# Kernel tuning notes

Hardware: AMD Instinct MI355X
Metric: run time of the kernel (lower is better)

The kernel has to match this reference:

```python
import jax, jax.numpy as jnp
import numpy as np

B, S, E, H = 1, 2048, 1024, 16
D = E // H
HEAVY_RATIO, RECENT_RATIO, PENALTY = 0.1, 0.1, 0.99
NEG = jnp.finfo(jnp.float32).min


def heavy_hitter_mask(attn, heavy_budget, recent_budget, penalty):
    # attn: [N, S, S] pre-softmax scores (with causal mask already added)
    N, Sq, _ = attn.shape
    cb = heavy_budget + recent_budget  # cache budget
    cols = jnp.arange(Sq)
    tmp = jax.nn.softmax(attn.astype(jnp.float32), axis=-1)
    # exponential penalty factor: penalty ** (cb-1, cb-2, ..., 0)
    pf = penalty ** (jnp.arange(cb, 0, -1).astype(jnp.float32) - 1.0)
    acc = jnp.einsum('nts,t->ns', tmp[:, :cb, :], pf)  # accumulated attention score [N,S]
    acc = acc * (cols < cb).astype(jnp.float32)        # zero beyond cache budget
    prev0 = jnp.broadcast_to(cols < cb, (N, Sq))       # mask_bottom row cb-1 (pre-tril)
    rows = jnp.swapaxes(attn[:, cb:, :], 0, 1)         # time-major [T,N,S]
    toks = jnp.arange(cb, Sq)

    def step(carry, inp):
        acc, prev = carry
        row, tok = inp
        li = tok - recent_budget                       # local_index
        in_local = (cols < li)[None, :]
        acc = jnp.where(in_local, acc * prev.astype(jnp.float32), acc)
        scores = jnp.where(in_local, acc, -jnp.inf)
        _, idx = jax.lax.top_k(scores, heavy_budget)   # heavy hitters [N,k]
        heavy = jnp.zeros((N, Sq), bool).at[jnp.arange(N)[:, None], idx].set(True)
        mask_row = heavy | (cols >= li)[None, :]
        p = jax.nn.softmax(jnp.where(mask_row, row.astype(jnp.float32), NEG), axis=-1)
        acc = acc * penalty + p
        # carry pre-tril row (matches torch loop); emit tril'd row
        return (acc, mask_row), mask_row & (cols <= tok)[None, :]

    (_, _), out_rows = jax.lax.scan(step, (acc, prev0), (rows, toks))
    # first cb rows: all-True cb x cb block, then tril -> causal within block
    top = jnp.broadcast_to((cols[None, :] <= jnp.arange(cb)[:, None])[None], (N, cb, Sq))
    return jnp.concatenate([top, jnp.swapaxes(out_rows, 0, 1)], axis=1)


def _forward(hidden_states, attention_mask, Wq, bq, Wk, bk, Wv, bv, Wo, bo):
    scaling = D ** -0.5
    q = (hidden_states @ Wq.T + bq) * scaling
    k = hidden_states @ Wk.T + bk
    v = hidden_states @ Wv.T + bv

    def shp(x):
        return x.reshape(B, S, H, D).transpose(0, 2, 1, 3).reshape(B * H, S, D)

    q, k, v = shp(q), shp(k), shp(v)
    attn = jnp.einsum('nsd,ntd->nst', q, k)                    # [B*H,S,S]
    attn = attn.reshape(B, H, S, S) + attention_mask
    attn = jnp.maximum(attn, NEG).reshape(B * H, S, S)
    hb = int(HEAVY_RATIO * S)
    rb = int(RECENT_RATIO * S)
    mask = heavy_hitter_mask(attn, hb, rb, PENALTY)
    attn = jnp.where(mask, attn, jnp.min(attention_mask))
    probs = jax.nn.softmax(attn.astype(jnp.float32), axis=-1)
    out = jnp.einsum('nst,ntd->nsd', probs, v)
    out = out.reshape(B, H, S, D).transpose(0, 2, 1, 3).reshape(B, S, E)
    return out @ Wo.T + bo


def setup_inputs() -> dict:
    key = jax.random.key(0)
    ks = jax.random.split(key, 9)
    hidden_states = jax.random.normal(ks[0], (B, S, E), jnp.float32)
    cols = jnp.arange(S)
    causal = (cols[None, :] <= cols[:, None])
    attention_mask = jnp.where(causal, 0.0, NEG)[None, None].astype(jnp.float32)
    attention_mask = jnp.broadcast_to(attention_mask, (B, 1, S, S)) + jnp.zeros((B, 1, S, S), jnp.float32)
    lin = lambda k: jax.random.normal(k, (E, E), jnp.float32) * 0.02
    return {
        'hidden_states': hidden_states,
        'attention_mask': attention_mask,
        'Wq': lin(ks[1]), 'bq': jnp.zeros((E,), jnp.float32),
        'Wk': lin(ks[2]), 'bk': jnp.zeros((E,), jnp.float32),
        'Wv': lin(ks[3]), 'bv': jnp.zeros((E,), jnp.float32),
        'Wo': lin(ks[4]), 'bo': jnp.zeros((E,), jnp.float32),
    }


def reference(hidden_states, attention_mask, Wq, bq, Wk, bk, Wv, bv, Wo, bo):
    return _forward(hidden_states, attention_mask, Wq, bq, Wk, bk, Wv, bv, Wo, bo)
```

## Files before the change

### kernel.cpp

```cpp
#include <hip/hip_runtime.h>

#define S_ 2048
#define E_ 1024
#define H_ 16
#define D_ 64
#define HB_ 204
#define RB_ 204
#define CB_ 408
#define NSCAN_ (S_ - CB_)
#define PEN_ 0.99f
#define NEGINF (-__builtin_huge_valf())
#define POSINF (__builtin_huge_valf())

typedef unsigned short u16;
typedef unsigned int u32;
typedef unsigned int u32x4 __attribute__((ext_vector_type(4)));

__device__ __forceinline__ float bf2f(u16 u) {
    union { u32 u; float f; } a; a.u = ((u32)u) << 16; return a.f;
}
__device__ __forceinline__ u16 f2bf(float f) {
    union { float f; u32 u; } a; a.f = f;
    u32 r = (a.u + 0x7FFFu + ((a.u >> 16) & 1u)) >> 16;
    return (u16)r;
}

#define DPPF(ID, V, CTRL, RMASK) \
    __int_as_float(__builtin_amdgcn_update_dpp(__float_as_int(ID), __float_as_int(V), CTRL, RMASK, 0xf, false))

__device__ __forceinline__ float wsum64_63(float v) {
    float t;
    t = DPPF(0.f, v, 0x111, 0xf); v += t;
    t = DPPF(0.f, v, 0x112, 0xf); v += t;
    t = DPPF(0.f, v, 0x114, 0xf); v += t;
    t = DPPF(0.f, v, 0x118, 0xf); v += t;
    t = DPPF(0.f, v, 0x142, 0xa); v += t;
    t = DPPF(0.f, v, 0x143, 0xc); v += t;
    return v;
}
__device__ __forceinline__ float wsum64(float v) {
    v = wsum64_63(v);
    return __int_as_float(__builtin_amdgcn_readlane(__float_as_int(v), 63));
}
template <int CTRL, int RMASK>
__device__ __forceinline__ double dmin_step(double v) {
    const int lo = __double2loint(v), hi = __double2hiint(v);
    const int slo = __builtin_amdgcn_update_dpp(0, lo, CTRL, RMASK, 0xf, false);
    const int shi = __builtin_amdgcn_update_dpp(0x7FF00000, hi, CTRL, RMASK, 0xf, false);
    return fmin(v, __hiloint2double(shi, slo));
}
__device__ __forceinline__ double wmind64(double v) {
    v = dmin_step<0x111, 0xf>(v);
    v = dmin_step<0x112, 0xf>(v);
    v = dmin_step<0x114, 0xf>(v);
    v = dmin_step<0x118, 0xf>(v);
    v = dmin_step<0x142, 0xa>(v);
    v = dmin_step<0x143, 0xc>(v);
    return v;
}

__global__ __launch_bounds__(256) void qkv_gemm(
    const float* __restrict__ X,
    const float* __restrict__ W0, const float* __restrict__ b0,
    const float* __restrict__ W1, const float* __restrict__ b1,
    const float* __restrict__ W2, const float* __restrict__ b2,
    float* __restrict__ Q, float* __restrict__ K, float* __restrict__ V)
{
    const int z = blockIdx.z;
    const float* W    = (z == 0) ? W0 : (z == 1) ? W1 : W2;
    const float* bias = (z == 0) ? b0 : (z == 1) ? b1 : b2;
    float* dst        = (z == 0) ? Q  : (z == 1) ? K  : V;
    const int o0 = blockIdx.x * 128, s0 = blockIdx.y * 128;
    __shared__ float As[16][132];
    __shared__ float Bs[16][132];
    const int tid = threadIdx.x;
    const int ty = tid >> 4, tx = tid & 15;
    const int r = tid >> 1, kq = (tid & 1) << 3;
    float acc[8][8] = {};
    for (int kb = 0; kb < E_; kb += 16) {
        float4 a0 = *(const float4*)&X[(size_t)(s0 + r) * E_ + kb + kq];
        float4 a1 = *(const float4*)&X[(size_t)(s0 + r) * E_ + kb + kq + 4];
        float4 w0 = *(const float4*)&W[(size_t)(o0 + r) * E_ + kb + kq];
        float4 w1 = *(const float4*)&W[(size_t)(o0 + r) * E_ + kb + kq + 4];
        __syncthreads();
        As[kq+0][r]=a0.x; As[kq+1][r]=a0.y; As[kq+2][r]=a0.z; As[kq+3][r]=a0.w;
        As[kq+4][r]=a1.x; As[kq+5][r]=a1.y; As[kq+6][r]=a1.z; As[kq+7][r]=a1.w;
        Bs[kq+0][r]=w0.x; Bs[kq+1][r]=w0.y; Bs[kq+2][r]=w0.z; Bs[kq+3][r]=w0.w;
        Bs[kq+4][r]=w1.x; Bs[kq+5][r]=w1.y; Bs[kq+6][r]=w1.z; Bs[kq+7][r]=w1.w;
        __syncthreads();
        #pragma unroll
        for (int kk = 0; kk < 16; ++kk) {
            float av[8], bv[8];
            *(float4*)&av[0] = *(const float4*)&As[kk][ty * 8];
            *(float4*)&av[4] = *(const float4*)&As[kk][ty * 8 + 4];
            *(float4*)&bv[0] = *(const float4*)&Bs[kk][tx * 8];
            *(float4*)&bv[4] = *(const float4*)&Bs[kk][tx * 8 + 4];
            #pragma unroll
            for (int i = 0; i < 8; ++i)
                #pragma unroll
                for (int j = 0; j < 8; ++j) acc[i][j] += av[i] * bv[j];
        }
    }
    #pragma unroll
    for (int i = 0; i < 8; ++i) {
        const int s = s0 + ty * 8 + i;
        #pragma unroll
        for (int jq = 0; jq < 2; ++jq) {
            const int o = o0 + tx * 8 + jq * 4;
            float4 v;
            v.x = acc[i][jq*4+0] + bias[o+0];
            v.y = acc[i][jq*4+1] + bias[o+1];
            v.z = acc[i][jq*4+2] + bias[o+2];
            v.w = acc[i][jq*4+3] + bias[o+3];
            if (z == 0) { v.x *= 0.125f; v.y *= 0.125f; v.z *= 0.125f; v.w *= 0.125f; }
            *(float4*)&dst[((size_t)(o >> 6) * S_ + s) * D_ + (o & 63)] = v;
        }
    }
}

__global__ __launch_bounds__(256) void proj_gemm(
    const float* __restrict__ X, const float* __restrict__ W,
    const float* __restrict__ bias, float* __restrict__ Y)
{
    const int o0 = blockIdx.x * 128, s0 = blockIdx.y * 128;
    __shared__ float As[16][132];
    __shared__ float Bs[16][132];
    const int tid = threadIdx.x;
    const int ty = tid >> 4, tx = tid & 15;
    const int r = tid >> 1, kq = (tid & 1) << 3;
    float acc[8][8] = {};
    for (int kb = 0; kb < E_; kb += 16) {
        float4 a0 = *(const float4*)&X[(size_t)(s0 + r) * E_ + kb + kq];
        float4 a1 = *(const float4*)&X[(size_t)(s0 + r) * E_ + kb + kq + 4];
        float4 w0 = *(const float4*)&W[(size_t)(o0 + r) * E_ + kb + kq];
        float4 w1 = *(const float4*)&W[(size_t)(o0 + r) * E_ + kb + kq + 4];
        __syncthreads();
        As[kq+0][r]=a0.x; As[kq+1][r]=a0.y; As[kq+2][r]=a0.z; As[kq+3][r]=a0.w;
        As[kq+4][r]=a1.x; As[kq+5][r]=a1.y; As[kq+6][r]=a1.z; As[kq+7][r]=a1.w;
        Bs[kq+0][r]=w0.x; Bs[kq+1][r]=w0.y; Bs[kq+2][r]=w0.z; Bs[kq+3][r]=w0.w;
        Bs[kq+4][r]=w1.x; Bs[kq+5][r]=w1.y; Bs[kq+6][r]=w1.z; Bs[kq+7][r]=w1.w;
        __syncthreads();
        #pragma unroll
        for (int kk = 0; kk < 16; ++kk) {
            float av[8], bv[8];
            *(float4*)&av[0] = *(const float4*)&As[kk][ty * 8];
            *(float4*)&av[4] = *(const float4*)&As[kk][ty * 8 + 4];
            *(float4*)&bv[0] = *(const float4*)&Bs[kk][tx * 8];
            *(float4*)&bv[4] = *(const float4*)&Bs[kk][tx * 8 + 4];
            #pragma unroll
            for (int i = 0; i < 8; ++i)
                #pragma unroll
                for (int j = 0; j < 8; ++j) acc[i][j] += av[i] * bv[j];
        }
    }
    #pragma unroll
    for (int i = 0; i < 8; ++i) {
        const int s = s0 + ty * 8 + i;
        #pragma unroll
        for (int jq = 0; jq < 2; ++jq) {
            const int o = o0 + tx * 8 + jq * 4;
            float4 v;
            v.x = acc[i][jq*4+0] + bias[o+0];
            v.y = acc[i][jq*4+1] + bias[o+1];
            v.z = acc[i][jq*4+2] + bias[o+2];
            v.w = acc[i][jq*4+3] + bias[o+3];
            *(float4*)&Y[(size_t)s * E_ + o] = v;
        }
    }
}

__global__ __launch_bounds__(256) void sc_gemm(const float* __restrict__ Q,
                                               const float* __restrict__ K,
                                               u16* __restrict__ Sc)
{
    const int h = blockIdx.z;
    const int jt = blockIdx.x, it = blockIdx.y;
    if (jt > it) return;
    const int i0 = it * 64, j0 = jt * 64;
    __shared__ float Qs[64][65];
    __shared__ float Ks[64][65];
    const float* Qh = Q + (size_t)h * S_ * D_;
    const float* Kh = K + (size_t)h * S_ * D_;
    const int tid = threadIdx.x;
    for (int idx = tid; idx < 1024; idx += 256) {
        const int rr = idx >> 4, c4 = (idx & 15) << 2;
        float4 q4 = *(const float4*)&Qh[(size_t)(i0 + rr) * D_ + c4];
        Qs[c4 + 0][rr] = q4.x; Qs[c4 + 1][rr] = q4.y; Qs[c4 + 2][rr] = q4.z; Qs[c4 + 3][rr] = q4.w;
        float4 k4 = *(const float4*)&Kh[(size_t)(j0 + rr) * D_ + c4];
        Ks[c4 + 0][rr] = k4.x; Ks[c4 + 1][rr] = k4.y; Ks[c4 + 2][rr] = k4.z; Ks[c4 + 3][rr] = k4.w;
    }
    __syncthreads();
    const int ty = tid >> 4, tx = tid & 15;
    float acc[4][4] = {};
    #pragma unroll 4
    for (int kk = 0; kk < 64; ++kk) {
        float4 a4 = *(const float4*)&Qs[kk][ty * 4];
        float4 b4 = *(const float4*)&Ks[kk][tx * 4];
        const float av[4] = {a4.x, a4.y, a4.z, a4.w};
        const float bv[4] = {b4.x, b4.y, b4.z, b4.w};
        #pragma unroll
        for (int i = 0; i < 4; ++i)
            #pragma unroll
            for (int j = 0; j < 4; ++j) acc[i][j] += av[i] * bv[j];
    }
    u16* out = Sc + ((size_t)h * S_ + i0) * S_ + j0;
    #pragma unroll
    for (int i = 0; i < 4; ++i)
        #pragma unroll
        for (int j = 0; j < 4; ++j)
            out[(size_t)(ty * 4 + i) * S_ + tx * 4 + j] = f2bf(acc[i][j]);
}

__global__ __launch_bounds__(256) void prep_kernel(const u16* __restrict__ Sc,
                                                   float* __restrict__ rsumG,
                                                   float* __restrict__ accG)
{
    const int h = blockIdx.y;
    const int wave = threadIdx.x >> 6, lane = threadIdx.x & 63;
    const int bx = blockIdx.x;
    if (bx < NSCAN_ / 4) {
        const int tok = CB_ + bx * 4 + wave;
        const u16* row = Sc + ((size_t)h * S_ + tok) * S_ + (tok - RB_);
        float sm = 0.f;
        #pragma unroll
        for (int k = 0; k < 4; ++k) {
            const int j = k * 64 + lane;
            if (j <= RB_) sm += __expf(bf2f(row[j]));
        }
        const float z = wsum64(sm);
        if (lane == 0) rsumG[(size_t)h * NSCAN_ + tok - CB_] = z;
    } else {
        const int t = (bx - NSCAN_ / 4) * 4 + wave;
        const u16* row = Sc + ((size_t)h * S_ + t) * S_;
        float sm = 0.f;
        for (int c = lane; c <= t; c += 64) sm += __expf(bf2f(row[c]));
        const float z = wsum64(sm);
        const float w = __powf(PEN_, (float)(CB_ - 1 - t)) / z;
        for (int c = lane; c <= t; c += 64)
            atomicAdd(&accG[h * CB_ + c], __expf(bf2f(row[c])) * w);
    }
}

#define NFULL_ (CB_ * H_)
#define NPART_ (NSCAN_ * H_)

__global__ __launch_bounds__(256) void scan_fill(const u16* __restrict__ Sc,
                                                 const float* __restrict__ accG,
                                                 const float* __restrict__ rsumG,
                                                 u16* __restrict__ heavyOut,
                                                 const float* __restrict__ V,
                                                 float* __restrict__ O)
{
    __shared__ __align__(16) char ldsPool[19984];
    const int bid = blockIdx.x;
    const int tid = threadIdx.x;

    if (bid >= 16) {
        float* sbuf  = (float*)ldsPool;
        float* wred  = (float*)(ldsPool + 1664);
        float* opart = (float*)(ldsPool + 1696);
        const int lane = tid & 63, wave = tid >> 6;
        int h, r, c0, n;
        bool partial;
        if (bid < 16 + NFULL_) {
            const int t2 = bid - 16;
            r = t2 >> 4; h = t2 & 15;
            c0 = 0; n = r + 1; partial = false;
        } else {
            const int idx = bid - 16 - NFULL_;
            r = CB_ + (idx >> 4); h = idx & 15;
            c0 = r - RB_; n = RB_ + 1; partial = true;
        }
        const u16* srow = Sc + ((size_t)h * S_ + r) * S_;
        float ls = 0.f;
        for (int i = tid; i < n; i += 256) {
            const float p = __expf(bf2f(srow[c0 + i]));
            sbuf[i] = p; ls += p;
        }
        ls = wsum64(ls);
        if (lane == 0) wred[wave] = ls;
        __syncthreads();
        const float Z = wred[0] + wred[1] + wred[2] + wred[3];
        float pv = 0.f;
        const float* vh = V + (size_t)h * S_ * D_;
        for (int i = wave; i < n; i += 4)
            pv += sbuf[i] * vh[(size_t)(c0 + i) * D_ + lane];
        opart[wave * 64 + lane] = pv;
        __syncthreads();
        if (tid < 64) {
            const float tot = opart[tid] + opart[64 + tid] + opart[128 + tid] + opart[192 + tid];
            O[(size_t)r * E_ + h * D_ + tid] = partial ? tot : (tot / Z);
        }
        return;
    }

    __builtin_amdgcn_s_setprio(3);
    const int h = bid;
    const int lane = tid & 63, wv = tid >> 6;
    float*  ring    = (float*)ldsPool;
    float*  rsumLDS = (float*)(ldsPool + 1024);
    u16*    buf_0   = (u16*)(ldsPool + 7584);
    u16*    buf_1   = (u16*)(ldsPool + 11680);
    u16*    buf_2   = (u16*)(ldsPool + 15776);
    float*  wredL   = (float*)(ldsPool + 19872);
    double* kredL   = (double*)(ldsPool + 19904);
    float*  el1L    = (float*)(ldsPool + 19968);
    const u16* sch = Sc + (size_t)h * S_ * S_;
    const float* accH = accG + h * CB_;
    u16* hOutH = heavyOut + (size_t)h * NSCAN_ * HB_;

    const bool vHeavy = (tid < HB_);
    const bool vRing  = (tid <= RB_);
    const bool vCand  = (tid == 255);

    u32x4 p0, p1, p2, p3;
    #define ISSUE1(BUF, ROWI)                                                 \
        do {                                                                  \
            const void* _ap = (const void*)((const char*)(sch + (size_t)(ROWI) * S_) + tid * 16); \
            asm volatile("global_load_dwordx4 %0, %1, off"                    \
                         : "=&v"(BUF) : "v"(_ap) : "memory");                 \
        } while (0)
    #define WAIT_VM(N) asm volatile("s_waitcnt vmcnt(" #N ")" ::: "memory")
    #define SBAR() asm volatile("s_waitcnt lgkmcnt(0)\n\ts_barrier" ::: "memory")

    ISSUE1(p0, CB_ + 0);
    ISSUE1(p1, CB_ + 1);
    ISSUE1(p2, CB_ + 2);
    ISSUE1(p3, CB_ + 3);

    for (int i = tid; i < NSCAN_; i += 256) rsumLDS[i] = rsumG[(size_t)h * NSCAN_ + i];
    for (int c = HB_ + tid; c < CB_; c += 256) ring[c & 255] = accH[c];
    int   hcol = vHeavy ? tid : 0;
    float hacc = vHeavy ? accH[tid] : POSINF;
    float accc;

    __syncthreads();
    ((u32x4*)buf_0)[tid] = p0;
    __syncthreads();

    {
        ISSUE1(p0, CB_ + 4);
        const u16* srow = buf_0;
        const float sg = bf2f(srow[hcol]);
        const float e  = vHeavy ? __expf(sg) : 0.f;
        const float ls = wsum64_63(e);
        if (lane == 63) wredL[wv] = ls;
        float oldw = 0.f, expw = 0.f;
        if (vRing) {
            expw = __expf(bf2f(srow[HB_ + tid]));
            oldw = (tid == RB_) ? 0.f : ring[(HB_ + tid) & 255];
        }
        ((u32x4*)buf_1)[tid] = p1;
        __syncthreads();
        const float4 ws = *(const float4*)wredL;
        const float Z = ws.x + ws.y + ws.z + ws.w + rsumLDS[0];
        const float invZ = __fdividef(1.f, Z);
        hacc = hacc * PEN_ + e * invZ;
        if (vHeavy) hOutH[tid] = (u16)tid;
        if (vRing)  ring[(HB_ + tid) & 255] = oldw * PEN_ + expw * invZ;
        __syncthreads();
        accc = ring[HB_ & 255];
    }

    #define SCAN_ITER(TOK, LD, ST, SB, DB, P)                                    \
    do {                                                                         \
        const int _si_tok = (TOK);                                               \
        const int _si_li  = _si_tok - RB_;                                       \
        const int _si_nr  = (_si_tok + 4 < S_) ? _si_tok + 4 : S_ - 1;           \
        ISSUE1(LD, _si_nr);                                                      \
        const u16* _si_srow = buf_##SB;                                          \
        const int   _si_hc = vCand ? (_si_li - 1) : hcol;                        \
        const float _si_ha = vCand ? accc : hacc;                                \
        const float _si_sg = bf2f(_si_srow[_si_hc]);                             \
        float _si_expw = 0.f;                                                    \
        if (vRing) _si_expw = __expf(bf2f(_si_srow[_si_li + tid]));              \
        const float _si_e = (vHeavy || vCand) ? __expf(_si_sg) : 0.f;            \
        const float _si_ls = wsum64_63(_si_e);                                   \
        double _si_key = __hiloint2double(__float_as_int(_si_ha),                \
                                          ((2047 - _si_hc) << 8) | tid);         \
        _si_key = wmind64(_si_key);                                              \
        if (lane == 63) {                                                        \
            wredL[(P) * 4 + wv] = _si_ls;                                        \
            kredL[(P) * 4 + wv] = _si_key;                                       \
            if (wv == 3) el1L[P] = _si_e;                                        \
        }                                                                        \
        WAIT_VM(3);                                                              \
        ((u32x4*)buf_##DB)[tid] = (ST);                                          \
        SBAR();                                                                  \
        const float4 _si_ws = *(const float4*)&wredL[(P) * 4];                   \
        const double _si_km = fmin(fmin(kredL[(P)*4+0], kredL[(P)*4+1]),         \
                                   fmin(kredL[(P)*4+2], kredL[(P)*4+3]));        \
        const int _si_lo  = __double2loint(_si_km);                              \
        const int _si_ev  = _si_lo & 255;                                        \
        const int _si_hev = 2047 - (_si_lo >> 8);                                \
        const float _si_ebc = __expf(bf2f(_si_srow[_si_hev]));                   \
        const float _si_el1 = el1L[P];                                           \
        const float _si_rsum = rsumLDS[_si_tok - CB_];                           \
        const float _si_Z = (_si_ws.x + _si_ws.y + _si_ws.z + _si_ws.w)          \
                            - _si_ebc + _si_rsum;                                \
        const float _si_invZ = __fdividef(1.f, _si_Z);                           \
        const float _si_oldw0 = ring[_si_li & 255];                              \
        if (vRing && tid != 0) {                                                 \
            const float _si_oldw = (tid == RB_) ? 0.f : ring[(_si_li + tid) & 255]; \
            ring[(_si_li + tid) & 255] = _si_oldw * PEN_ + _si_expw * _si_invZ;  \
        }                                                                        \
        const bool _si_m = (tid == _si_ev);                                      \
        hcol = _si_m ? (_si_li - 1) : _si_hc;                                    \
        hacc = (_si_m ? accc : _si_ha) * PEN_                                    \
             + (_si_m ? _si_el1 : _si_e) * _si_invZ;                             \
        const float _si_ew0 = __expf(bf2f(_si_srow[_si_li]));                    \
        accc = _si_oldw0 * PEN_ + _si_ew0 * _si_invZ;                            \
        if (vHeavy) hOutH[(size_t)(_si_tok - CB_) * HB_ + tid] = (u16)hcol;      \
    } while (0)

    SCAN_ITER(CB_ + 1, p1, p2, 1, 2, 1);
    SCAN_ITER(CB_ + 2, p2, p3, 2, 0, 0);
    SCAN_ITER(CB_ + 3, p3, p0, 0, 1, 1);
    SCAN_ITER(CB_ + 4, p0, p1, 1, 2, 0);
    for (int t = CB_ + 5; t + 11 <= S_ - 4; t += 12) {
        SCAN_ITER(t + 0,  p1, p2, 2, 0, 1);
        SCAN_ITER(t + 1,  p2, p3, 0, 1, 0);
        SCAN_ITER(t + 2,  p3, p0, 1, 2, 1);
        SCAN_ITER(t + 3,  p0, p1, 2, 0, 0);
        SCAN_ITER(t + 4,  p1, p2, 0, 1, 1);
        SCAN_ITER(t + 5,  p2, p3, 1, 2, 0);
        SCAN_ITER(t + 6,  p3, p0, 2, 0, 1);
        SCAN_ITER(t + 7,  p0, p1, 0, 1, 0);
        SCAN_ITER(t + 8,  p1, p2, 1, 2, 1);
        SCAN_ITER(t + 9,  p2, p3, 2, 0, 0);
        SCAN_ITER(t + 10, p3, p0, 0, 1, 1);
        SCAN_ITER(t + 11, p0, p1, 1, 2, 0);
    }
    SCAN_ITER(S_ - 3, p1, p2, 2, 0, 1);
    SCAN_ITER(S_ - 2, p2, p3, 0, 1, 0);
    SCAN_ITER(S_ - 1, p3, p0, 1, 2, 1);
    #undef SCAN_ITER
    #undef ISSUE1
    #undef WAIT_VM
    #undef SBAR
}

__global__ __launch_bounds__(256) void heavy_merge(const u16* __restrict__ Sc,
                                                   const float* __restrict__ V,
                                                   const u16* __restrict__ heavyIn,
                                                   const float* __restrict__ rsumG,
                                                   float* __restrict__ O)
{
    const int idx = blockIdx.x;
    const int r = CB_ + (idx >> 4), h = idx & 15;
    const int tid = threadIdx.x;
    const int lane = tid & 63, wave = tid >> 6;
    __shared__ float sbuf[208];
    __shared__ u16 cbuf[208];
    __shared__ float wred[4];
    __shared__ float opart[4][64];
    const u16* srow = Sc + ((size_t)h * S_ + r) * S_;
    const u16* hrow = heavyIn + ((size_t)h * NSCAN_ + (r - CB_)) * HB_;
    float ls = 0.f;
    for (int i = tid; i < HB_; i += 256) {
        const int col = hrow[i];
        const float p = __expf(bf2f(srow[col]));
        sbuf[i] = p; cbuf[i] = (u16)col;
        ls += p;
    }
    ls = wsum64(ls);
    if (lane == 0) wred[wave] = ls;
    __syncthreads();
    const float Z = wred[0] + wred[1] + wred[2] + wred[3]
                  + rsumG[(size_t)h * NSCAN_ + r - CB_];
    float pv = 0.f;
    const float* vh = V + (size_t)h * S_ * D_;
    for (int i = wave; i < HB_; i += 4)
        pv += sbuf[i] * vh[(size_t)cbuf[i] * D_ + lane];
    opart[wave][lane] = pv;
    __syncthreads();
    if (tid < 64) {
        const float tot = opart[0][tid] + opart[1][tid] + opart[2][tid] + opart[3][tid];
        float* op = &O[(size_t)r * E_ + h * D_ + tid];
        *op = (*op + tot) / Z;
    }
}

extern "C" void kernel_launch(void* const* d_in, const int* in_sizes, int n_in,
                              void* d_out, int out_size, void* d_ws, size_t ws_size,
                              hipStream_t stream)
{
    const float* hs = (const float*)d_in[0];
    const float* Wq = (const float*)d_in[2];
    const float* bq = (const float*)d_in[3];
    const float* Wk = (const float*)d_in[4];
    const float* bk = (const float*)d_in[5];
    const float* Wv = (const float*)d_in[6];
    const float* bv = (const float*)d_in[7];
    const float* Wo = (const float*)d_in[8];
    const float* bo = (const float*)d_in[9];

    char* ws = (char*)d_ws;
    const size_t MB = 1024 * 1024;
    float* Q     = (float*)(ws);
    float* K     = (float*)(ws + 8 * MB);
    float* V     = (float*)(ws + 16 * MB);
    u16*   Sc    = (u16*)  (ws + 24 * MB);
    u16*   hvy   = (u16*)  (ws + 152 * MB);
    float* rsumG = (float*)(ws + 163 * MB);
    float* accG  = (float*)(ws + 164 * MB);
    float* O     = (float*)(ws + 168 * MB);
    (void)ws_size; (void)in_sizes; (void)n_in; (void)out_size;

    (void)hipMemsetAsync(accG, 0, (size_t)H_ * CB_ * sizeof(float), stream);
    qkv_gemm<<<dim3(8, 16, 3), 256, 0, stream>>>(hs, Wq, bq, Wk, bk, Wv, bv, Q, K, V);
    sc_gemm <<<dim3(32, 32, 16), 256, 0, stream>>>(Q, K, Sc);
    prep_kernel<<<dim3(NSCAN_ / 4 + CB_ / 4, H_), 256, 0, stream>>>(Sc, rsumG, accG);
    scan_fill<<<16 + NFULL_ + NPART_, 256, 0, stream>>>(Sc, accG, rsumG, hvy, V, O);
    heavy_merge<<<NPART_, 256, 0, stream>>>(Sc, V, hvy, rsumG, O);
    proj_gemm<<<dim3(8, 16, 1), 256, 0, stream>>>(O, Wo, bo, (float*)d_out);
}
```

Baseline: 1.637 ms.

## Software-pipeline heavy-hitter scan with speculative next-row sums and min-payload reduction

Restructures the sequential per-head scan so each step computes the next row's exponentials and partial sums speculatively, then corrects the sum after the evicted index is known. The argmin reduction now carries the evicted element's exp value as a payload, which removes the dependent LDS reload of the evicted column. The row prefetch is deepened and a ramp phase is added. The goal is to shorten the serial critical path per token and get one barrier per step. In exchange it uses more LDS and carries more registers and bookkeeping, and the speculative correction adds risk of subtle numerical or indexing mismatches.

```diff
diff --git a/kernel.cpp b/kernel.cpp
--- a/kernel.cpp
+++ b/kernel.cpp
@@ -57,6 +57,23 @@
     v = dmin_step<0x142, 0xa>(v);
     v = dmin_step<0x143, 0xc>(v);
     return v;
+}
+template <int CTRL, int RMASK>
+__device__ __forceinline__ void dminp_step(double& v, float& p) {
+    const int lo = __double2loint(v), hi = __double2hiint(v);
+    const int slo = __builtin_amdgcn_update_dpp(0, lo, CTRL, RMASK, 0xf, false);
+    const int shi = __builtin_amdgcn_update_dpp(0x7FF00000, hi, CTRL, RMASK, 0xf, false);
+    const int spi = __builtin_amdgcn_update_dpp(0, __float_as_int(p), CTRL, RMASK, 0xf, false);
+    const double sv = __hiloint2double(shi, slo);
+    if (sv < v) { v = sv; p = __int_as_float(spi); }
+}
+__device__ __forceinline__ void wminp64(double& v, float& p) {
+    dminp_step<0x111, 0xf>(v, p);
+    dminp_step<0x112, 0xf>(v, p);
+    dminp_step<0x114, 0xf>(v, p);
+    dminp_step<0x118, 0xf>(v, p);
+    dminp_step<0x142, 0xa>(v, p);
+    dminp_step<0x143, 0xc>(v, p);
 }
 
 __global__ __launch_bounds__(256) void qkv_gemm(
@@ -251,7 +268,7 @@
                                                  const float* __restrict__ V,
                                                  float* __restrict__ O)
 {
-    __shared__ __align__(16) char ldsPool[19984];
+    __shared__ __align__(16) char ldsPool[22112];
     const int bid = blockIdx.x;
     const int tid = threadIdx.x;
 
@@ -302,9 +319,13 @@
     u16*    buf_0   = (u16*)(ldsPool + 7584);
     u16*    buf_1   = (u16*)(ldsPool + 11680);
     u16*    buf_2   = (u16*)(ldsPool + 15776);
-    float*  wredL   = (float*)(ldsPool + 19872);
-    double* kredL   = (double*)(ldsPool + 19904);
-    float*  el1L    = (float*)(ldsPool + 19968);
+    float*  esL     = (float*)(ldsPool + 19872);
+    double* kredL   = (double*)(ldsPool + 21920);
+    float*  payL    = (float*)(ldsPool + 21984);
+    float*  SspecL  = (float*)(ldsPool + 22016);
+    float*  wredL   = (float*)(ldsPool + 22048);
+    float*  el1L    = (float*)(ldsPool + 22080);
+    float*  sredL   = (float*)(ldsPool + 22088);
     const u16* sch = Sc + (size_t)h * S_ * S_;
     const float* accH = accG + h * CB_;
     u16* hOutH = heavyOut + (size_t)h * NSCAN_ * HB_;
@@ -333,13 +354,19 @@
     int   hcol = vHeavy ? tid : 0;
     float hacc = vHeavy ? accH[tid] : POSINF;
     float accc;
+    float e_prev, es_spec, el1_prev, ew0_prev, ec1_cur, ec255_cur, ew0_cur;
+    float expw_prev, S_prev, rsum_prev;
 
     __syncthreads();
     ((u32x4*)buf_0)[tid] = p0;
+    ((u32x4*)buf_1)[tid] = p1;
+    ISSUE1(p0, CB_ + 4);
+    ISSUE1(p1, CB_ + 5);
     __syncthreads();
 
     {
-        ISSUE1(p0, CB_ + 4);
+        ((u32x4*)buf_2)[tid] = p2;
+        ISSUE1(p2, CB_ + 6);
         const u16* srow = buf_0;
         const float sg = bf2f(srow[hcol]);
         const float e  = vHeavy ? __expf(sg) : 0.f;
@@ -350,7 +377,6 @@
             expw = __expf(bf2f(srow[HB_ + tid]));
             oldw = (tid == RB_) ? 0.f : ring[(HB_ + tid) & 255];
         }
-        ((u32x4*)buf_1)[tid] = p1;
         __syncthreads();
         const float4 ws = *(const float4*)wredL;
         const float Z = ws.x + ws.y + ws.z + ws.w + rsumLDS[0];
@@ -362,12 +388,12 @@
         accc = ring[HB_ & 255];
     }
 
-    #define SCAN_ITER(TOK, LD, ST, SB, DB, P)                                    \
+    #define RAMP_ITER(TOK, RG, SB, DB, P)                                        \
     do {                                                                         \
         const int _si_tok = (TOK);                                               \
         const int _si_li  = _si_tok - RB_;                                       \
-        const int _si_nr  = (_si_tok + 4 < S_) ? _si_tok + 4 : S_ - 1;           \
-        ISSUE1(LD, _si_nr);                                                      \
+        ((u32x4*)buf_##DB)[tid] = RG;             \
+        ISSUE1(RG, _si_tok + 6);                                                 \
         const u16* _si_srow = buf_##SB;                                          \
         const int   _si_hc = vCand ? (_si_li - 1) : hcol;                        \
         const float _si_ha = vCand ? accc : hacc;                                \
@@ -380,14 +406,12 @@
                                           ((2047 - _si_hc) << 8) | tid);         \
         _si_key = wmind64(_si_key);                                              \
         if (lane == 63) {                                                        \
-            wredL[(P) * 4 + wv] = _si_ls;                                        \
-            kredL[(P) * 4 + wv] = _si_key;                                       \
+            wredL[(P)*4+wv] = _si_ls;                                            \
+            kredL[(P)*4+wv] = _si_key;                                           \
             if (wv == 3) el1L[P] = _si_e;                                        \
         }                                                                        \
-        WAIT_VM(3);                                                              \
-        ((u32x4*)buf_##DB)[tid] = (ST);                                          \
-        SBAR();                                                                  \
-        const float4 _si_ws = *(const float4*)&wredL[(P) * 4];                   \
+        __syncthreads();                                                         \
+        const float4 _si_ws = *(const float4*)&wredL[(P)*4];                     \
         const double _si_km = fmin(fmin(kredL[(P)*4+0], kredL[(P)*4+1]),         \
                                    fmin(kredL[(P)*4+2], kredL[(P)*4+3]));        \
         const int _si_lo  = __double2loint(_si_km);                              \
@@ -411,30 +435,145 @@
         const float _si_ew0 = __expf(bf2f(_si_srow[_si_li]));                    \
         accc = _si_oldw0 * PEN_ + _si_ew0 * _si_invZ;                            \
         if (vHeavy) hOutH[(size_t)(_si_tok - CB_) * HB_ + tid] = (u16)hcol;      \
+        __syncthreads();                                                         \
     } while (0)
 
-    SCAN_ITER(CB_ + 1, p1, p2, 1, 2, 1);
-    SCAN_ITER(CB_ + 2, p2, p3, 2, 0, 0);
-    SCAN_ITER(CB_ + 3, p3, p0, 0, 1, 1);
-    SCAN_ITER(CB_ + 4, p0, p1, 1, 2, 0);
-    for (int t = CB_ + 5; t + 11 <= S_ - 4; t += 12) {
-        SCAN_ITER(t + 0,  p1, p2, 2, 0, 1);
-        SCAN_ITER(t + 1,  p2, p3, 0, 1, 0);
-        SCAN_ITER(t + 2,  p3, p0, 1, 2, 1);
-        SCAN_ITER(t + 3,  p0, p1, 2, 0, 0);
-        SCAN_ITER(t + 4,  p1, p2, 0, 1, 1);
-        SCAN_ITER(t + 5,  p2, p3, 1, 2, 0);
-        SCAN_ITER(t + 6,  p3, p0, 2, 0, 1);
-        SCAN_ITER(t + 7,  p0, p1, 0, 1, 0);
-        SCAN_ITER(t + 8,  p1, p2, 1, 2, 1);
-        SCAN_ITER(t + 9,  p2, p3, 2, 0, 0);
-        SCAN_ITER(t + 10, p3, p0, 0, 1, 1);
-        SCAN_ITER(t + 11, p0, p1, 1, 2, 0);
-    }
-    SCAN_ITER(S_ - 3, p1, p2, 2, 0, 1);
-    SCAN_ITER(S_ - 2, p2, p3, 0, 1, 0);
-    SCAN_ITER(S_ - 1, p3, p0, 1, 2, 1);
-    #undef SCAN_ITER
+    RAMP_ITER(CB_ + 1, p3, 1, 0, 1);
+    RAMP_ITER(CB_ + 2, p0, 2, 1, 0);
+    RAMP_ITER(CB_ + 3, p1, 0, 2, 1);
+    RAMP_ITER(CB_ + 4, p2, 1, 0, 0);
+    #undef RAMP_ITER
+
+    {
+        const int t = CB_ + 5;
+        const int liC = t - RB_;
+        const u16* rowT = buf_2;
+        const u16* rowN = buf_0;
+        ((u32x4*)buf_1)[tid] = p3;
+        ISSUE1(p3, t + 6);
+        float eC;
+        if (vHeavy)      eC = __expf(bf2f(rowT[hcol]));
+        else if (vCand)  eC = __expf(bf2f(rowT[liC - 1]));
+        else             eC = 0.f;
+        const int   hc = vCand ? (liC - 1) : hcol;
+        const float ha = vCand ? accc : hacc;
+        double key = __hiloint2double(__float_as_int(ha), ((2047 - hc) << 8) | tid);
+        float pay = eC;
+        wminp64(key, pay);
+        if (lane == 63) { kredL[4 + wv] = key; payL[4 + wv] = pay; }
+        const float ls = wsum64_63(eC);
+        if (lane == 63) sredL[wv] = ls;
+        const float ec1N   = __expf(bf2f(rowN[liC - 1]));
+        const float ec255N = __expf(bf2f(rowN[liC]));
+        const float ew0N   = __expf(bf2f(rowN[liC + 1]));
+        float esN;
+        if (vHeavy)      esN = __expf(bf2f(rowN[hcol]));
+        else if (vCand)  esN = ec255N;
+        else             esN = 0.f;
+        esL[256 + tid] = esN;
+        const float ls2 = wsum64_63(esN);
+        if (lane == 63) SspecL[4 + wv] = ls2;
+        el1_prev  = __expf(bf2f(rowT[liC - 1]));
+        ew0_prev  = __expf(bf2f(rowT[liC]));
+        expw_prev = vRing ? __expf(bf2f(rowT[liC + tid])) : 0.f;
+        e_prev = eC; es_spec = esN;
+        ec1_cur = ec1N; ec255_cur = ec255N; ew0_cur = ew0N;
+        rsum_prev = rsumLDS[t - CB_];
+        __syncthreads();
+        S_prev = sredL[0] + sredL[1] + sredL[2] + sredL[3];
+    }
+
+    #define SBODY(TOK, RG, SB0, SB1, DB, P)                                      \
+    do {                                                                         \
+        const int _t   = (TOK);                                                  \
+        const int _liP = _t - RB_ - 1;                                           \
+        const int _liC = _t - RB_;                                               \
+        WAIT_VM(3);                                                              \
+        ((u32x4*)buf_##DB)[tid] = RG;                                            \
+        ISSUE1(RG, (_t + 6 < S_) ? _t + 6 : S_ - 1);                             \
+        const u16* _rowT = buf_##SB0;                                            \
+        const u16* _rowN = buf_##SB1;                                            \
+        double _k0 = kredL[(1-(P))*4+0], _k1 = kredL[(1-(P))*4+1];               \
+        double _k2 = kredL[(1-(P))*4+2], _k3 = kredL[(1-(P))*4+3];               \
+        float _q0 = payL[(1-(P))*4+0], _q1 = payL[(1-(P))*4+1];                  \
+        float _q2 = payL[(1-(P))*4+2], _q3 = payL[(1-(P))*4+3];                  \
+        const float4 _w4 = *(const float4*)&SspecL[(1-(P))*4];                   \
+        float _oldw = 0.f;                                                       \
+        if (vRing) _oldw = (tid == RB_) ? 0.f : ring[(_liP + tid) & 255];        \
+        const float _oldw0 = ring[_liP & 255];                                   \
+        const float _rs = rsumLDS[_t - CB_];                                     \
+        double _km = _k0; float _pm = _q0;                                       \
+        if (_k1 < _km) { _km = _k1; _pm = _q1; }                                 \
+        if (_k2 < _km) { _km = _k2; _pm = _q2; }                                 \
+        if (_k3 < _km) { _km = _k3; _pm = _q3; }                                 \
+        const int _ev = __double2loint(_km) & 255;                               \
+        const float _Z = S_prev - _pm + rsum_prev;                               \
+        const float _invZ = __fdividef(1.f, _Z);                                 \
+        const bool _m = (tid == _ev);                                            \
+        hacc = (_m ? accc : hacc) * PEN_ + (_m ? el1_prev : e_prev) * _invZ;     \
+        if (_m && _ev != 255) hcol = _liP - 1;                                   \
+        const float _acccN = _oldw0 * PEN_ + ew0_prev * _invZ;                   \
+        if (vRing && tid != 0)                                                   \
+            ring[(_liP + tid) & 255] = _oldw * PEN_ + expw_prev * _invZ;         \
+        if (vHeavy) hOutH[(size_t)(_t - 1 - CB_) * HB_ + tid] = (u16)hcol;       \
+        accc = _acccN;                                                           \
+        const float _eC = (_m && _ev != 255) ? ec1_cur : es_spec;                \
+        float _sc = 0.f;                                                         \
+        if (_ev != 255) _sc = ec1_cur - esL[(1-(P))*256 + _ev];                  \
+        const float _S = _w4.x + _w4.y + _w4.z + _w4.w + _sc;                    \
+        const int   _hc = vCand ? (_liC - 1) : hcol;                             \
+        const float _ha = vCand ? accc : hacc;                                   \
+        double _key = __hiloint2double(__float_as_int(_ha),                      \
+                                       ((2047 - _hc) << 8) | tid);               \
+        float _pay = _eC;                                                        \
+        wminp64(_key, _pay);                                                     \
+        if (lane == 63) { kredL[(P)*4+wv] = _key; payL[(P)*4+wv] = _pay; }       \
+        const float _ec1N   = __expf(bf2f(_rowN[_liC - 1]));                     \
+        const float _ec255N = __expf(bf2f(_rowN[_liC]));                         \
+        const float _ew0N   = __expf(bf2f(_rowN[_liC + 1]));                     \
+        float _esN;                                                              \
+        if (vHeavy)      _esN = __expf(bf2f(_rowN[hcol]));                       \
+        else if (vCand)  _esN = _ec255N;                                         \
+        else             _esN = 0.f;                                             \
+        esL[(P)*256 + tid] = _esN;                                               \
+        const float _ls = wsum64_63(_esN);                                       \
+        if (lane == 63) SspecL[(P)*4+wv] = _ls;                                  \
+        const float _expwC = vRing ? __expf(bf2f(_rowT[_liC + tid])) : 0.f;      \
+        e_prev = _eC; es_spec = _esN;                                            \
+        el1_prev = ec255_cur; ew0_prev = ew0_cur;                                \
+        ec1_cur = _ec1N; ec255_cur = _ec255N; ew0_cur = _ew0N;                   \
+        expw_prev = _expwC; S_prev = _S; rsum_prev = _rs;                        \
+        SBAR();                                                                  \
+    } while (0)
+
+    for (int t0 = CB_ + 6; t0 + 11 <= S_ - 3; t0 += 12) {
+        SBODY(t0 + 0,  p0, 0, 1, 2, 0);
+        SBODY(t0 + 1,  p1, 1, 2, 0, 1);
+        SBODY(t0 + 2,  p2, 2, 0, 1, 0);
+        SBODY(t0 + 3,  p3, 0, 1, 2, 1);
+        SBODY(t0 + 4,  p0, 1, 2, 0, 0);
+        SBODY(t0 + 5,  p1, 2, 0, 1, 1);
+        SBODY(t0 + 6,  p2, 0, 1, 2, 0);
+        SBODY(t0 + 7,  p3, 1, 2, 0, 1);
+        SBODY(t0 + 8,  p0, 2, 0, 1, 0);
+        SBODY(t0 + 9,  p1, 0, 1, 2, 1);
+        SBODY(t0 + 10, p2, 1, 2, 0, 0);
+        SBODY(t0 + 11, p3, 2, 0, 1, 1);
+    }
+    SBODY(S_ - 2, p0, 0, 1, 2, 0);
+    SBODY(S_ - 1, p1, 1, 2, 0, 1);
+    #undef SBODY
+
+    {
+        double k0 = kredL[4], k1 = kredL[5], k2 = kredL[6], k3 = kredL[7];
+        double km = k0;
+        if (k1 < km) km = k1;
+        if (k2 < km) km = k2;
+        if (k3 < km) km = k3;
+        const int ev = __double2loint(km) & 255;
+        if (tid == ev && ev != 255) hcol = (S_ - 1 - RB_) - 1;
+        if (vHeavy) hOutH[(size_t)(S_ - 1 - CB_) * HB_ + tid] = (u16)hcol;
+    }
     #undef ISSUE1
     #undef WAIT_VM
     #undef SBAR
```

After: 1.925 ms. +17.6%, slower.

## Software-pipeline heavy-hitter scan: prefetch next-row exps and carry evicted payload in reduction

Applied to the files above, without the earlier changes.

Restructures the serial per-token scan so each step computes the next row's exponentials after its single barrier, leaving them ready for the following step. The evicted element's exp value now travels with the min-key through the wave and block reductions (wminp64 with a payload), which removes the dependent LDS read plus exp after the barrier. Prefetch depth grows from 4 to 6 rows, using a three-buffer rotation and a few warm-up steps with two barriers each. This shortens the critical path of the serial scan, at the cost of more registers, more DPP ops and more complex buffer bookkeeping.

```diff
diff --git a/kernel.cpp b/kernel.cpp
--- a/kernel.cpp
+++ b/kernel.cpp
@@ -57,6 +57,23 @@
     v = dmin_step<0x142, 0xa>(v);
     v = dmin_step<0x143, 0xc>(v);
     return v;
+}
+template <int CTRL, int RMASK>
+__device__ __forceinline__ void dminp_step(double& v, float& p) {
+    const int lo = __double2loint(v), hi = __double2hiint(v);
+    const int slo = __builtin_amdgcn_update_dpp(0, lo, CTRL, RMASK, 0xf, false);
+    const int shi = __builtin_amdgcn_update_dpp(0x7FF00000, hi, CTRL, RMASK, 0xf, false);
+    const int spi = __builtin_amdgcn_update_dpp(0, __float_as_int(p), CTRL, RMASK, 0xf, false);
+    const double sv = __hiloint2double(shi, slo);
+    if (sv < v) { v = sv; p = __int_as_float(spi); }
+}
+__device__ __forceinline__ void wminp64(double& v, float& p) {
+    dminp_step<0x111, 0xf>(v, p);
+    dminp_step<0x112, 0xf>(v, p);
+    dminp_step<0x114, 0xf>(v, p);
+    dminp_step<0x118, 0xf>(v, p);
+    dminp_step<0x142, 0xa>(v, p);
+    dminp_step<0x143, 0xc>(v, p);
 }
 
 __global__ __launch_bounds__(256) void qkv_gemm(
@@ -251,7 +268,7 @@
                                                  const float* __restrict__ V,
                                                  float* __restrict__ O)
 {
-    __shared__ __align__(16) char ldsPool[19984];
+    __shared__ __align__(16) char ldsPool[20096];
     const int bid = blockIdx.x;
     const int tid = threadIdx.x;
 
@@ -304,7 +321,8 @@
     u16*    buf_2   = (u16*)(ldsPool + 15776);
     float*  wredL   = (float*)(ldsPool + 19872);
     double* kredL   = (double*)(ldsPool + 19904);
-    float*  el1L    = (float*)(ldsPool + 19968);
+    float*  payL    = (float*)(ldsPool + 19968);
+    float*  el1L    = (float*)(ldsPool + 20000);
     const u16* sch = Sc + (size_t)h * S_ * S_;
     const float* accH = accG + h * CB_;
     u16* hOutH = heavyOut + (size_t)h * NSCAN_ * HB_;
@@ -333,13 +351,18 @@
     int   hcol = vHeavy ? tid : 0;
     float hacc = vHeavy ? accH[tid] : POSINF;
     float accc;
+    float e_cur, el1_cur, ew0_cur, expw_cur, rsum_cur;
 
     __syncthreads();
     ((u32x4*)buf_0)[tid] = p0;
+    ISSUE1(p0, CB_ + 4);
+    ((u32x4*)buf_1)[tid] = p1;
+    ISSUE1(p1, CB_ + 5);
     __syncthreads();
 
     {
-        ISSUE1(p0, CB_ + 4);
+        ((u32x4*)buf_2)[tid] = p2;
+        ISSUE1(p2, CB_ + 6);
         const u16* srow = buf_0;
         const float sg = bf2f(srow[hcol]);
         const float e  = vHeavy ? __expf(sg) : 0.f;
@@ -350,7 +373,6 @@
             expw = __expf(bf2f(srow[HB_ + tid]));
             oldw = (tid == RB_) ? 0.f : ring[(HB_ + tid) & 255];
         }
-        ((u32x4*)buf_1)[tid] = p1;
         __syncthreads();
         const float4 ws = *(const float4*)wredL;
         const float Z = ws.x + ws.y + ws.z + ws.w + rsumLDS[0];
@@ -362,79 +384,151 @@
         accc = ring[HB_ & 255];
     }
 
-    #define SCAN_ITER(TOK, LD, ST, SB, DB, P)                                    \
+    #define RSTEP(TOK, Q, DBUF, SBUF, P)                                         \
     do {                                                                         \
-        const int _si_tok = (TOK);                                               \
-        const int _si_li  = _si_tok - RB_;                                       \
-        const int _si_nr  = (_si_tok + 4 < S_) ? _si_tok + 4 : S_ - 1;           \
-        ISSUE1(LD, _si_nr);                                                      \
-        const u16* _si_srow = buf_##SB;                                          \
-        const int   _si_hc = vCand ? (_si_li - 1) : hcol;                        \
-        const float _si_ha = vCand ? accc : hacc;                                \
-        const float _si_sg = bf2f(_si_srow[_si_hc]);                             \
-        float _si_expw = 0.f;                                                    \
-        if (vRing) _si_expw = __expf(bf2f(_si_srow[_si_li + tid]));              \
-        const float _si_e = (vHeavy || vCand) ? __expf(_si_sg) : 0.f;            \
-        const float _si_ls = wsum64_63(_si_e);                                   \
-        double _si_key = __hiloint2double(__float_as_int(_si_ha),                \
-                                          ((2047 - _si_hc) << 8) | tid);         \
-        _si_key = wmind64(_si_key);                                              \
+        const int _t  = (TOK);                                                   \
+        const int _li = _t - RB_;                                                \
+        asm volatile("s_waitcnt vmcnt(0)" ::: "memory");                         \
+        ((u32x4*)(DBUF))[tid] = Q;                                               \
+        ISSUE1(Q, _t + 6);                                                       \
+        const u16* _sr = (const u16*)(SBUF);                                     \
+        const int   _hc = vCand ? (_li - 1) : hcol;                              \
+        const float _ha = vCand ? accc : hacc;                                   \
+        const float _sg = bf2f(_sr[_hc]);                                        \
+        float _expw = 0.f;                                                       \
+        if (vRing) _expw = __expf(bf2f(_sr[_li + tid]));                         \
+        const float _e = (vHeavy || vCand) ? __expf(_sg) : 0.f;                  \
+        const float _ls = wsum64_63(_e);                                         \
+        double _key = __hiloint2double(__float_as_int(_ha),                      \
+                                       ((2047 - _hc) << 8) | tid);               \
+        _key = wmind64(_key);                                                    \
         if (lane == 63) {                                                        \
-            wredL[(P) * 4 + wv] = _si_ls;                                        \
-            kredL[(P) * 4 + wv] = _si_key;                                       \
-            if (wv == 3) el1L[P] = _si_e;                                        \
+            wredL[(P)*4+wv] = _ls;                                               \
+            kredL[(P)*4+wv] = _key;                                              \
+            if (wv == 3) el1L[P] = _e;                                           \
         }                                                                        \
-        WAIT_VM(3);                                                              \
-        ((u32x4*)buf_##DB)[tid] = (ST);                                          \
+        __syncthreads();                                                         \
+        const float4 _w4 = *(const float4*)&wredL[(P)*4];                        \
+        const double _km = fmin(fmin(kredL[(P)*4+0], kredL[(P)*4+1]),            \
+                                fmin(kredL[(P)*4+2], kredL[(P)*4+3]));           \
+        const int _lo  = __double2loint(_km);                                    \
+        const int _ev  = _lo & 255;                                              \
+        const int _hev = 2047 - (_lo >> 8);                                      \
+        const float _ebc = __expf(bf2f(_sr[_hev]));                              \
+        const float _el1 = el1L[P];                                              \
+        const float _rs = rsumLDS[_t - CB_];                                     \
+        const float _Z = (_w4.x + _w4.y + _w4.z + _w4.w) - _ebc + _rs;           \
+        const float _invZ = __fdividef(1.f, _Z);                                 \
+        const float _oldw0 = ring[_li & 255];                                    \
+        if (vRing && tid != 0) {                                                 \
+            const float _oldw = (tid == RB_) ? 0.f : ring[(_li + tid) & 255];    \
+            ring[(_li + tid) & 255] = _oldw * PEN_ + _expw * _invZ;              \
+        }                                                                        \
+        const bool _m = (tid == _ev);                                            \
+        hcol = _m ? (_li - 1) : _hc;                                             \
+        hacc = (_m ? accc : _ha) * PEN_ + (_m ? _el1 : _e) * _invZ;              \
+        const float _ew0 = __expf(bf2f(_sr[_li]));                               \
+        accc = _oldw0 * PEN_ + _ew0 * _invZ;                                     \
+        if (vHeavy) hOutH[(size_t)(_t - CB_) * HB_ + tid] = (u16)hcol;           \
+        __syncthreads();                                                         \
+    } while (0)
+
+    RSTEP(CB_ + 1, p3, buf_0, buf_1, 1);
+    RSTEP(CB_ + 2, p0, buf_1, buf_2, 0);
+    RSTEP(CB_ + 3, p1, buf_2, buf_0, 1);
+    RSTEP(CB_ + 4, p2, buf_0, buf_1, 0);
+    #undef RSTEP
+
+    {
+        const u16* rt = buf_2;
+        const int li = CB_ + 5 - RB_;
+        const float fixC = __expf(bf2f(rt[li - 1]));
+        const float sg = bf2f(rt[hcol]);
+        e_cur   = vCand ? fixC : (vHeavy ? __expf(sg) : 0.f);
+        el1_cur = fixC;
+        ew0_cur = __expf(bf2f(rt[li]));
+        expw_cur = vRing ? __expf(bf2f(rt[li + tid])) : 0.f;
+        rsum_cur = rsumLDS[CB_ + 5 - CB_];
+    }
+
+    #define STEP(TOK, Q, DBUF, SNBUF, P)                                         \
+    do {                                                                         \
+        const int _t  = (TOK);                                                   \
+        const int _li = _t - RB_;                                                \
+        if (_t + 2 < S_) {                                                       \
+            WAIT_VM(3);                                                          \
+            ((u32x4*)(DBUF))[tid] = Q;                                           \
+            ISSUE1(Q, (_t + 6 < S_) ? _t + 6 : S_ - 1);                          \
+        }                                                                        \
+        const float _ls = wsum64_63(e_cur);                                      \
+        const int   _kc = vCand ? (_li - 1) : hcol;                              \
+        const float _ka = vCand ? accc : hacc;                                   \
+        double _key = __hiloint2double(__float_as_int(_ka),                      \
+                                       ((2047 - _kc) << 8) | tid);               \
+        float _pay = e_cur;                                                      \
+        wminp64(_key, _pay);                                                     \
+        if (lane == 63) {                                                        \
+            wredL[(P)*4+wv] = _ls;                                               \
+            kredL[(P)*4+wv] = _key;                                              \
+            payL[(P)*4+wv]  = _pay;                                              \
+        }                                                                        \
         SBAR();                                                                  \
-        const float4 _si_ws = *(const float4*)&wredL[(P) * 4];                   \
-        const double _si_km = fmin(fmin(kredL[(P)*4+0], kredL[(P)*4+1]),         \
-                                   fmin(kredL[(P)*4+2], kredL[(P)*4+3]));        \
-        const int _si_lo  = __double2loint(_si_km);                              \
-        const int _si_ev  = _si_lo & 255;                                        \
-        const int _si_hev = 2047 - (_si_lo >> 8);                                \
-        const float _si_ebc = __expf(bf2f(_si_srow[_si_hev]));                   \
-        const float _si_el1 = el1L[P];                                           \
-        const float _si_rsum = rsumLDS[_si_tok - CB_];                           \
-        const float _si_Z = (_si_ws.x + _si_ws.y + _si_ws.z + _si_ws.w)          \
-                            - _si_ebc + _si_rsum;                                \
-        const float _si_invZ = __fdividef(1.f, _si_Z);                           \
-        const float _si_oldw0 = ring[_si_li & 255];                              \
-        if (vRing && tid != 0) {                                                 \
-            const float _si_oldw = (tid == RB_) ? 0.f : ring[(_si_li + tid) & 255]; \
-            ring[(_si_li + tid) & 255] = _si_oldw * PEN_ + _si_expw * _si_invZ;  \
-        }                                                                        \
-        const bool _si_m = (tid == _si_ev);                                      \
-        hcol = _si_m ? (_si_li - 1) : _si_hc;                                    \
-        hacc = (_si_m ? accc : _si_ha) * PEN_                                    \
-             + (_si_m ? _si_el1 : _si_e) * _si_invZ;                             \
-        const float _si_ew0 = __expf(bf2f(_si_srow[_si_li]));                    \
-        accc = _si_oldw0 * PEN_ + _si_ew0 * _si_invZ;                            \
-        if (vHeavy) hOutH[(size_t)(_si_tok - CB_) * HB_ + tid] = (u16)hcol;      \
+        const u16* _rn = (const u16*)(SNBUF);                                    \
+        const u16 _sgq  = _rn[_kc & 2047];                                       \
+        const u16 _sgE  = _rn[(_li - 1) & 2047];                                 \
+        const u16 _sgC  = _rn[_li & 2047];                                       \
+        const u16 _sgW0 = _rn[(_li + 1) & 2047];                                 \
+        const u16 _sgRW = _rn[(_li + 1 + tid) & 2047];                           \
+        const float4 _w4 = *(const float4*)&wredL[(P)*4];                        \
+        double _k0 = kredL[(P)*4+0], _k1 = kredL[(P)*4+1];                       \
+        double _k2 = kredL[(P)*4+2], _k3 = kredL[(P)*4+3];                       \
+        float  _q0 = payL[(P)*4+0], _q1 = payL[(P)*4+1];                         \
+        float  _q2 = payL[(P)*4+2], _q3 = payL[(P)*4+3];                         \
+        const float _oldw0 = ring[_li & 255];                                    \
+        float _oldw = 0.f;                                                       \
+        if (vRing) _oldw = (tid == RB_) ? 0.f : ring[(_li + tid) & 255];         \
+        double _km = _k0; float _pm = _q0;                                       \
+        if (_k1 < _km) { _km = _k1; _pm = _q1; }                                 \
+        if (_k2 < _km) { _km = _k2; _pm = _q2; }                                 \
+        if (_k3 < _km) { _km = _k3; _pm = _q3; }                                 \
+        const int _ev = __double2loint(_km) & 255;                               \
+        const float _Z = _w4.x + _w4.y + _w4.z + _w4.w - _pm + rsum_cur;         \
+        const float _invZ = __fdividef(1.f, _Z);                                 \
+        const bool _m = (tid == _ev);                                            \
+        hacc = (_m ? accc : _ka) * PEN_ + (_m ? el1_cur : e_cur) * _invZ;        \
+        hcol = _m ? (_li - 1) : _kc;                                             \
+        if (vRing && tid != 0)                                                   \
+            ring[(_li + tid) & 255] = _oldw * PEN_ + expw_cur * _invZ;           \
+        accc = _oldw0 * PEN_ + ew0_cur * _invZ;                                  \
+        if (vHeavy) hOutH[(size_t)(_t - CB_) * HB_ + tid] = (u16)hcol;           \
+        const float _eS = __expf(bf2f(_sgq));                                    \
+        const float _eE = __expf(bf2f(_sgE));                                    \
+        const float _eC = __expf(bf2f(_sgC));                                    \
+        e_cur   = vCand ? _eC : (vHeavy ? (_m ? _eE : _eS) : 0.f);               \
+        el1_cur = _eC;                                                           \
+        ew0_cur = __expf(bf2f(_sgW0));                                           \
+        expw_cur = vRing ? __expf(bf2f(_sgRW)) : 0.f;                            \
+        rsum_cur = (_t + 1 - CB_ < NSCAN_) ? rsumLDS[_t + 1 - CB_] : 0.f;        \
     } while (0)
 
-    SCAN_ITER(CB_ + 1, p1, p2, 1, 2, 1);
-    SCAN_ITER(CB_ + 2, p2, p3, 2, 0, 0);
-    SCAN_ITER(CB_ + 3, p3, p0, 0, 1, 1);
-    SCAN_ITER(CB_ + 4, p0, p1, 1, 2, 0);
-    for (int t = CB_ + 5; t + 11 <= S_ - 4; t += 12) {
-        SCAN_ITER(t + 0,  p1, p2, 2, 0, 1);
-        SCAN_ITER(t + 1,  p2, p3, 0, 1, 0);
-        SCAN_ITER(t + 2,  p3, p0, 1, 2, 1);
-        SCAN_ITER(t + 3,  p0, p1, 2, 0, 0);
-        SCAN_ITER(t + 4,  p1, p2, 0, 1, 1);
-        SCAN_ITER(t + 5,  p2, p3, 1, 2, 0);
-        SCAN_ITER(t + 6,  p3, p0, 2, 0, 1);
-        SCAN_ITER(t + 7,  p0, p1, 0, 1, 0);
-        SCAN_ITER(t + 8,  p1, p2, 1, 2, 1);
-        SCAN_ITER(t + 9,  p2, p3, 2, 0, 0);
-        SCAN_ITER(t + 10, p3, p0, 0, 1, 1);
-        SCAN_ITER(t + 11, p0, p1, 1, 2, 0);
-    }
-    SCAN_ITER(S_ - 3, p1, p2, 2, 0, 1);
-    SCAN_ITER(S_ - 2, p2, p3, 0, 1, 0);
-    SCAN_ITER(S_ - 1, p3, p0, 1, 2, 1);
-    #undef SCAN_ITER
+    for (int t0 = CB_ + 5; t0 + 11 <= S_ - 4; t0 += 12) {
+        STEP(t0 + 0,  p3, buf_1, buf_0, 1);
+        STEP(t0 + 1,  p0, buf_2, buf_1, 0);
+        STEP(t0 + 2,  p1, buf_0, buf_2, 1);
+        STEP(t0 + 3,  p2, buf_1, buf_0, 0);
+        STEP(t0 + 4,  p3, buf_2, buf_1, 1);
+        STEP(t0 + 5,  p0, buf_0, buf_2, 0);
+        STEP(t0 + 6,  p1, buf_1, buf_0, 1);
+        STEP(t0 + 7,  p2, buf_2, buf_1, 0);
+        STEP(t0 + 8,  p3, buf_0, buf_2, 1);
+        STEP(t0 + 9,  p0, buf_1, buf_0, 0);
+        STEP(t0 + 10, p1, buf_2, buf_1, 1);
+        STEP(t0 + 11, p2, buf_0, buf_2, 0);
+    }
+    STEP(S_ - 3, p3, buf_1, buf_0, 1);
+    STEP(S_ - 2, p0, buf_2, buf_1, 0);
+    STEP(S_ - 1, p1, buf_0, buf_2, 1);
+    #undef STEP
     #undef ISSUE1
     #undef WAIT_VM
     #undef SBAR
```

After: 1.765 ms. +7.8%, slower.
